# Optimization experiments

Hardware: AMD Instinct MI355X
Metric: run time of the kernel (lower is better)

Reference implementation:

```python
import jax, jax.numpy as jnp
import numpy as np

FIELDS = 39
FEATURE_DIMS = 100000
EMB = 16


def setup_inputs() -> dict:
    key = jax.random.key(0)
    k1, k2 = jax.random.split(key)
    X = jax.random.randint(k1, (4096, FIELDS), 0, FEATURE_DIMS, dtype=jnp.int32)
    table = jax.random.normal(k2, (FEATURE_DIMS, FIELDS, EMB), dtype=jnp.float32) * 0.05
    return {"X": X, "table": table}


def reference(X, table):
    # FFM field-aware interaction, strict upper triangle of field pairs.
    # Original builds full [B,F,F,D] product then masks; math per pair (i<j):
    #   out[b,p,d] = table[X[b,i], j, d] * table[X[b,j], i, d]
    F = FIELDS
    iu, ju = np.triu_indices(F, k=1)          # P = F*(F-1)//2 pairs
    left = table[X[:, iu], ju]                # [B, P, D]
    right = table[X[:, ju], iu]               # [B, P, D]
    return left * right
```

## Files before the change

### kernel.cpp

```cpp
#include <hip/hip_runtime.h>


#define F       39
#define EMBF4   4
#define NPAIR   741
#define PPB     64

__global__ __launch_bounds__(256) void ffm_interact_kernel(
    const int* __restrict__ X,
    const float4* __restrict__ table4,
    float4* __restrict__ out4)
{
    __shared__ int xrow[F];
    const int b = blockIdx.y;
    if (threadIdx.x < F) xrow[threadIdx.x] = X[b * F + threadIdx.x];
    __syncthreads();

    const int lane_e = threadIdx.x & 3;
    const int p = blockIdx.x * PPB + (threadIdx.x >> 2);
    if (p >= NPAIR) return;

    int i = (int)((77.0f - sqrtf(5929.0f - 8.0f * (float)p)) * 0.5f);
    i = i < 0 ? 0 : (i > 38 ? 38 : i);
    while (((i + 1) * (77 - (i + 1))) / 2 <= p) ++i;
    while ((i * (77 - i)) / 2 > p) --i;
    const int j = p - (i * (77 - i)) / 2 + i + 1;

    const int ri = xrow[i];
    const int rj = xrow[j];

    const float4 L = table4[(ri * F + j) * EMBF4 + lane_e];
    const float4 R = table4[(rj * F + i) * EMBF4 + lane_e];

    float4 o;
    o.x = L.x * R.x;
    o.y = L.y * R.y;
    o.z = L.z * R.z;
    o.w = L.w * R.w;
    out4[(b * NPAIR + p) * EMBF4 + lane_e] = o;
}

extern "C" void kernel_launch(void* const* d_in, const int* in_sizes, int n_in,
                              void* d_out, int out_size, void* d_ws, size_t ws_size,
                              hipStream_t stream) {
    const int*   X     = (const int*)d_in[0];
    const float* table = (const float*)d_in[1];
    float*       out   = (float*)d_out;

    const int batch = in_sizes[0] / F;

    dim3 grid((NPAIR + PPB - 1) / PPB, batch);
    ffm_interact_kernel<<<grid, 256, 0, stream>>>(
        X, (const float4*)table, (float4*)out);
}
```

Measured before the change: 408.1 us.

## Stage per-sample embedding rows in LDS and compute all pairs per block

Each block now handles one batch sample, loading all 39 field rows of the table into shared memory with coalesced reads, precomputing pair offsets, then forming all 741 pair products from LDS with nontemporal stores. This replaces scattered 64-byte gathers from global memory with contiguous row loads. The large LDS footprint limits occupancy to one block per CU and serializes load and compute phases.

```diff
diff --git a/kernel.cpp b/kernel.cpp
--- a/kernel.cpp
+++ b/kernel.cpp
@@ -1,43 +1,57 @@
 #include <hip/hip_runtime.h>
+#include <math.h>
 
 
 #define F       39
-#define EMBF4   4
 #define NPAIR   741
-#define PPB     64
+#define ROWF4   (F * 4)
+#define OUTF4   (NPAIR * 4)
+#define BLK     1024
 
-__global__ __launch_bounds__(256) void ffm_interact_kernel(
+typedef float fx4 __attribute__((ext_vector_type(4)));
+
+__global__ __launch_bounds__(BLK) void ffm_interact_kernel(
     const int* __restrict__ X,
-    const float4* __restrict__ table4,
-    float4* __restrict__ out4)
+    const fx4* __restrict__ table4,
+    fx4*       __restrict__ out4)
 {
+    __shared__ fx4 rows[F * ROWF4];
     __shared__ int xrow[F];
-    const int b = blockIdx.y;
-    if (threadIdx.x < F) xrow[threadIdx.x] = X[b * F + threadIdx.x];
+    __shared__ int loff[NPAIR];
+    __shared__ int roff[NPAIR];
+
+    const int b   = blockIdx.x;
+    const int tid = threadIdx.x;
+
+    if (tid < F) xrow[tid] = X[b * F + tid];
+
+    if (tid < NPAIR) {
+        const int p = tid;
+        int i = (int)((77.0f - sqrtf(5929.0f - 8.0f * (float)p)) * 0.5f);
+        i = i < 0 ? 0 : (i > 38 ? 38 : i);
+        while (((i + 1) * (77 - (i + 1))) / 2 <= p) ++i;
+        while ((i * (77 - i)) / 2 > p) --i;
+        const int j = p - (i * (77 - i)) / 2 + i + 1;
+        loff[p] = i * ROWF4 + j * 4;
+        roff[p] = j * ROWF4 + i * 4;
+    }
     __syncthreads();
 
-    const int lane_e = threadIdx.x & 3;
-    const int p = blockIdx.x * PPB + (threadIdx.x >> 2);
-    if (p >= NPAIR) return;
+    for (int idx = tid; idx < F * ROWF4; idx += BLK) {
+        const int f = idx / ROWF4;
+        const int w = idx - f * ROWF4;
+        rows[idx] = table4[(size_t)xrow[f] * ROWF4 + w];
+    }
+    __syncthreads();
 
-    int i = (int)((77.0f - sqrtf(5929.0f - 8.0f * (float)p)) * 0.5f);
-    i = i < 0 ? 0 : (i > 38 ? 38 : i);
-    while (((i + 1) * (77 - (i + 1))) / 2 <= p) ++i;
-    while ((i * (77 - i)) / 2 > p) --i;
-    const int j = p - (i * (77 - i)) / 2 + i + 1;
-
-    const int ri = xrow[i];
-    const int rj = xrow[j];
-
-    const float4 L = table4[(ri * F + j) * EMBF4 + lane_e];
-    const float4 R = table4[(rj * F + i) * EMBF4 + lane_e];
-
-    float4 o;
-    o.x = L.x * R.x;
-    o.y = L.y * R.y;
-    o.z = L.z * R.z;
-    o.w = L.w * R.w;
-    out4[(b * NPAIR + p) * EMBF4 + lane_e] = o;
+    fx4* __restrict__ ob = out4 + (size_t)b * OUTF4;
+    for (int o = tid; o < OUTF4; o += BLK) {
+        const int p = o >> 2;
+        const int e = o & 3;
+        const fx4 L = rows[loff[p] + e];
+        const fx4 R = rows[roff[p] + e];
+        __builtin_nontemporal_store(L * R, ob + o);
+    }
 }
 
 extern "C" void kernel_launch(void* const* d_in, const int* in_sizes, int n_in,
@@ -49,7 +63,6 @@
 
     const int batch = in_sizes[0] / F;
 
-    dim3 grid((NPAIR + PPB - 1) / PPB, batch);
-    ffm_interact_kernel<<<grid, 256, 0, stream>>>(
-        X, (const float4*)table, (float4*)out);
+    ffm_interact_kernel<<<dim3(batch), dim3(BLK), 0, stream>>>(
+        X, (const fx4*)table, (fx4*)out);
 }
```

New measurement: 420.4 us. 1.03x slower.
